# Kernel tuning notes

Hardware: AMD Instinct MI355X
Metric: run time of the kernel (lower is better)

## Reference

```python
import jax, jax.numpy as jnp
import numpy as np

D_MODEL = 128
NHEAD = 8
NLAYERS = 6
LAYER_NAMES = ['self', 'cross', 'self', 'cross', 'self', 'cross']
TEMPERATURE = 5.0
EPS = 1e-6


def _pos_encoding(x):
    # Sinusoidal 1D position encoding along the width axis. x: [N, H, W, C]
    C, W = x.shape[-1], x.shape[2]
    pos = jnp.arange(W, dtype=x.dtype)[:, None]                      # [W,1]
    div = jnp.exp(jnp.arange(0, C, 2, dtype=x.dtype) * (-np.log(10000.0) / C))
    pe = jnp.zeros((W, C), x.dtype)
    pe = pe.at[:, 0::2].set(jnp.sin(pos * div))
    pe = pe.at[:, 1::2].set(jnp.cos(pos * div))
    return x + pe[None, None]                                        # broadcast over N,H


def _linear_attention(q, k, v):
    # q,k,v: [N, H, W, nhead, dim]; kernelized linear attention along W
    Q = jax.nn.elu(q) + 1.0
    K = jax.nn.elu(k) + 1.0
    v_len = v.shape[2]
    V = v / v_len
    KV = jnp.einsum('nhsed,nhsev->nhedv', K, V)                      # [N,H,e,d,d]
    Z = 1.0 / (jnp.einsum('nhled,nhed->nhle', Q, K.sum(axis=2)) + EPS)
    return jnp.einsum('nhled,nhedv,nhle->nhlev', Q, KV, Z) * v_len


def _layer_norm(x, g, b):
    m = x.mean(-1, keepdims=True)
    v = jnp.mean((x - m) ** 2, -1, keepdims=True)
    return (x - m) / jnp.sqrt(v + 1e-5) * g + b


def _encoder_layer(x, source, Wq, Wk, Wv, Wm, W1, W2, g1, b1, g2, b2):
    x = _pos_encoding(x)
    source = _pos_encoding(source)
    bs, h, w, c = x.shape
    e, d = NHEAD, c // NHEAD
    q = (x @ Wq).reshape(bs, h, w, e, d)
    k = (source @ Wk).reshape(bs, h, w, e, d)
    v = (source @ Wv).reshape(bs, h, w, e, d)
    msg = _linear_attention(q, k, v).reshape(bs, h, w, c) @ Wm
    msg = _layer_norm(msg, g1, b1)
    msg = jnp.concatenate([x, msg], axis=-1)                         # [N,H,W,2C]
    msg = jax.nn.relu(msg @ W1) @ W2
    msg = _layer_norm(msg, g2, b2)
    return x + msg


def _forward(feat0, feat1, Wq, Wk, Wv, Wm, W1, W2, g1, b1, g2, b2):
    feat0 = feat0.transpose(0, 2, 3, 1)                              # [N,H,W,C]
    feat1 = feat1.transpose(0, 2, 3, 1)
    for i, name in enumerate(LAYER_NAMES):
        p = (Wq[i], Wk[i], Wv[i], Wm[i], W1[i], W2[i], g1[i], b1[i], g2[i], b2[i])
        if name == 'self':
            feat0 = _encoder_layer(feat0, feat0, *p)
            feat1 = _encoder_layer(feat1, feat1, *p)
        else:  # cross: sequential update (feat1 sees updated feat0), as in torch source
            feat0 = _encoder_layer(feat0, feat1, *p)
            feat1 = _encoder_layer(feat1, feat0, *p)
    w = feat0.shape[2]
    attn_mask = jnp.where(jnp.triu(jnp.ones((w, w), bool), 1), -jnp.inf, 0.0)
    attn_mask = attn_mask[None, None].astype(feat0.dtype)
    scale = feat0.shape[-1] ** 0.5
    sim = jnp.einsum('ntwc,ntlc->ntwl', feat0 / scale, feat1 / scale) / TEMPERATURE
    return sim + attn_mask


def setup_inputs() -> dict:
    key = jax.random.key(0)
    ks = jax.random.split(key, 12)
    N, C, H, W = 2, D_MODEL, 64, 640
    L, D = NLAYERS, D_MODEL
    s = 1.0 / np.sqrt(D)
    s2 = 1.0 / np.sqrt(2 * D)
    return {
        'feat0': jax.random.normal(ks[0], (N, C, H, W), jnp.float32),
        'feat1': jax.random.normal(ks[1], (N, C, H, W), jnp.float32),
        'Wq': jax.random.normal(ks[2], (L, D, D), jnp.float32) * s,
        'Wk': jax.random.normal(ks[3], (L, D, D), jnp.float32) * s,
        'Wv': jax.random.normal(ks[4], (L, D, D), jnp.float32) * s,
        'Wm': jax.random.normal(ks[5], (L, D, D), jnp.float32) * s,
        'W1': jax.random.normal(ks[6], (L, 2 * D, 2 * D), jnp.float32) * s2,
        'W2': jax.random.normal(ks[7], (L, 2 * D, D), jnp.float32) * s2,
        'g1': jnp.ones((L, D), jnp.float32),
        'b1': jnp.zeros((L, D), jnp.float32),
        'g2': jnp.ones((L, D), jnp.float32),
        'b2': jnp.zeros((L, D), jnp.float32),
    }


def reference(feat0, feat1, Wq, Wk, Wv, Wm, W1, W2, g1, b1, g2, b2):
    return _forward(feat0, feat1, Wq, Wk, Wv, Wm, W1, W2, g1, b1, g2, b2)
```

## Files before the change

kernel.cpp:

```cpp
#include <hip/hip_runtime.h>
#include <cmath>
#include <math.h>

#define TOK 81920
#define WDIM 640

typedef __attribute__((ext_vector_type(8))) short short8v;
typedef __attribute__((ext_vector_type(4))) short short4v;
typedef __attribute__((ext_vector_type(4))) float f32x4;

__device__ __forceinline__ short f2bf(float f) {
  union { float f; unsigned u; } x; x.f = f;
  unsigned r = (x.u + 0x7fffu + ((x.u >> 16) & 1u)) >> 16;
  return (short)r;
}
__device__ __forceinline__ float bf2f(short s) {
  union { unsigned u; float f; } x; x.u = ((unsigned)(unsigned short)s) << 16;
  return x.f;
}

__global__ __launch_bounds__(256) void pe_kernel(float* __restrict__ pe) {
  int id = blockIdx.x * 256 + threadIdx.x;
  if (id >= WDIM * 128) return;
  int w = id >> 7;
  int c = id & 127;
  float i2 = (float)(c & 126);
  float freq = expf(i2 * -0.071955784156063941f);
  float ang = (float)w * freq;
  pe[id] = (c & 1) ? cosf(ang) : sinf(ang);
}

__global__ __launch_bounds__(256) void tr_kernel(const float* __restrict__ in0,
                                                 const float* __restrict__ in1,
                                                 short* __restrict__ x0,
                                                 short* __restrict__ x1) {
  __shared__ float t[32][33];
  int w0 = blockIdx.x * 32;
  int c0 = blockIdx.y * 32;
  int z = blockIdx.z;
  int feat = z >> 7;
  int nh = z & 127;
  int n = nh >> 6, h = nh & 63;
  const float* in = feat ? in1 : in0;
  short* out = feat ? x1 : x0;
  int tx = threadIdx.x & 31, ty = threadIdx.x >> 5;
  const float* ip = in + ((n * 128 + c0) * 64 + h) * 640 + w0;
#pragma unroll
  for (int i = 0; i < 32; i += 8)
    t[ty + i][tx] = ip[(ty + i) * (64 * 640) + tx];
  __syncthreads();
  short* op = out + ((size_t)(n * 64 + h) * 640 + w0) * 128 + c0;
#pragma unroll
  for (int i = 0; i < 32; i += 8)
    op[(size_t)(ty + i) * 128 + tx] = f2bf(t[tx][ty + i]);
}

__global__ __launch_bounds__(256) void wprep_kernel(
    const float* __restrict__ Wq, const float* __restrict__ Wk,
    const float* __restrict__ Wv, const float* __restrict__ Wm,
    const float* __restrict__ W1, const float* __restrict__ W2,
    short* __restrict__ BT) {
  int id = blockIdx.x * 256 + threadIdx.x;
  if (id >= 6 * 163840) return;
  int layer = id / 163840;
  int r = id % 163840;
  float v;
  if (r < 65536) {
    int seg = r >> 14;
    int rr = r & 16383;
    int n = rr >> 7, k = rr & 127;
    const float* W = seg == 0 ? Wq : seg == 1 ? Wk : seg == 2 ? Wv : Wm;
    v = W[layer * 16384 + k * 128 + n];
  } else if (r < 131072) {
    int rr = r - 65536;
    int n = rr >> 8, k = rr & 255;
    v = W1[layer * 65536 + k * 256 + n];
  } else {
    int rr = r - 131072;
    int n = rr >> 8, k = rr & 255;
    v = W2[layer * 32768 + k * 128 + n];
  }
  BT[id] = f2bf(v);
}

__device__ __forceinline__ void load_af(const short* __restrict__ A,
                                        const float* __restrict__ pe,
                                        int bm, int wr, int l15, int lk,
                                        short8v af[4][4]) {
  const int wbase = bm % WDIM;
#pragma unroll
  for (int mf = 0; mf < 4; ++mf) {
    const int rl = wr * 64 + mf * 16 + l15;
    const short* ar = A + (size_t)(bm + rl) * 128;
    const float* pr = pe + (size_t)(wbase + rl) * 128;
#pragma unroll
    for (int ks = 0; ks < 4; ++ks) {
      const int kloc = ks * 32 + lk * 8;
      short8v xa = *(const short8v*)(ar + kloc);
      f32x4 p0 = *(const f32x4*)(pr + kloc);
      f32x4 p1 = *(const f32x4*)(pr + kloc + 4);
      short8v o;
      o[0] = f2bf(bf2f(xa[0]) + p0[0]); o[1] = f2bf(bf2f(xa[1]) + p0[1]);
      o[2] = f2bf(bf2f(xa[2]) + p0[2]); o[3] = f2bf(bf2f(xa[3]) + p0[3]);
      o[4] = f2bf(bf2f(xa[4]) + p1[0]); o[5] = f2bf(bf2f(xa[5]) + p1[1]);
      o[6] = f2bf(bf2f(xa[6]) + p1[2]); o[7] = f2bf(bf2f(xa[7]) + p1[3]);
      af[ks][mf] = o;
    }
  }
}

__device__ __forceinline__ void proj_pass_T(const short8v af[4][4],
                                            const short* __restrict__ WT,
                                            int wr, int wc, int l15, int lk,
                                            short (*tS)[136]) {
  f32x4 acc[4][4] = {};
#pragma unroll
  for (int ks = 0; ks < 4; ++ks) {
    const int kloc = ks * 32 + lk * 8;
    short8v bfr[4];
#pragma unroll
    for (int nf = 0; nf < 4; ++nf)
      bfr[nf] = *(const short8v*)&WT[(size_t)(wc * 64 + nf * 16 + l15) * 128 + kloc];
#pragma unroll
    for (int mf = 0; mf < 4; ++mf)
#pragma unroll
      for (int nf = 0; nf < 4; ++nf)
        acc[mf][nf] = __builtin_amdgcn_mfma_f32_16x16x32_bf16(
            bfr[nf], af[ks][mf], acc[mf][nf], 0, 0, 0);
  }
#pragma unroll
  for (int mf = 0; mf < 4; ++mf)
#pragma unroll
    for (int nf = 0; nf < 4; ++nf) {
      short4v p;
      p[0] = f2bf(acc[mf][nf][0]); p[1] = f2bf(acc[mf][nf][1]);
      p[2] = f2bf(acc[mf][nf][2]); p[3] = f2bf(acc[mf][nf][3]);
      *(short4v*)&tS[wr * 64 + mf * 16 + l15][wc * 64 + nf * 16 + lk * 4] = p;
    }
}

__device__ __forceinline__ void tile_out(const short (*tS)[136], int bm, int tid,
                                         short* __restrict__ out) {
#pragma unroll
  for (int it = 0; it < 8; ++it) {
    int u = it * 256 + tid;
    int row = u >> 4, seg = u & 15;
    *(short8v*)&out[(size_t)(bm + row) * 128 + seg * 8] =
        *(const short8v*)&tS[row][seg * 8];
  }
}

__global__ __launch_bounds__(256) void qkv_self_kernel(
    const short* __restrict__ x0, const short* __restrict__ x1,
    const float* __restrict__ pe,
    const short* __restrict__ wqT, const short* __restrict__ wkT,
    const short* __restrict__ wvT,
    short* q0, short* k0, short* v0, short* q1, short* k1, short* v1) {
  __shared__ short tS[128][136];
  const int tid = threadIdx.x, lane = tid & 63, wid = tid >> 6;
  const int wr = wid >> 1, wc = wid & 1;
  const int bm = blockIdx.x * 128;
  const int l15 = lane & 15, lk = lane >> 4;
  const int z = blockIdx.z;
  const short* A = z ? x1 : x0;
  short8v af[4][4];
  load_af(A, pe, bm, wr, l15, lk, af);
  proj_pass_T(af, wqT, wr, wc, l15, lk, tS);
  __syncthreads();
  tile_out(tS, bm, tid, z ? q1 : q0);
  __syncthreads();
  proj_pass_T(af, wkT, wr, wc, l15, lk, tS);
  __syncthreads();
  tile_out(tS, bm, tid, z ? k1 : k0);
  __syncthreads();
  proj_pass_T(af, wvT, wr, wc, l15, lk, tS);
  __syncthreads();
  tile_out(tS, bm, tid, z ? v1 : v0);
}

__global__ __launch_bounds__(256) void qkv_cross_kernel(
    const short* __restrict__ xq, const short* __restrict__ xs,
    const float* __restrict__ pe,
    const short* __restrict__ wqT, const short* __restrict__ wkT,
    const short* __restrict__ wvT,
    short* qb, short* kb, short* vb) {
  __shared__ short tS[128][136];
  const int tid = threadIdx.x, lane = tid & 63, wid = tid >> 6;
  const int wr = wid >> 1, wc = wid & 1;
  const int bm = blockIdx.x * 128;
  const int l15 = lane & 15, lk = lane >> 4;
  short8v af[4][4];
  if (blockIdx.y == 0) {
    load_af(xq, pe, bm, wr, l15, lk, af);
    proj_pass_T(af, wqT, wr, wc, l15, lk, tS);
    __syncthreads();
    tile_out(tS, bm, tid, qb);
  } else {
    load_af(xs, pe, bm, wr, l15, lk, af);
    proj_pass_T(af, wkT, wr, wc, l15, lk, tS);
    __syncthreads();
    tile_out(tS, bm, tid, kb);
    __syncthreads();
    proj_pass_T(af, wvT, wr, wc, l15, lk, tS);
    __syncthreads();
    tile_out(tS, bm, tid, vb);
  }
}

template <int NSC>
__global__ __launch_bounds__(256) void kv_kernel(
    const short* __restrict__ k0, const short* __restrict__ v0,
    const short* __restrict__ k1, const short* __restrict__ v1,
    float* __restrict__ kvp) {
  const int bid = blockIdx.x;
  const int sc = bid % NSC;
  const int e = bid / NSC;
  const int strip = sc / 5, chunk = sc % 5;
  const short* kb = (strip >= 128) ? k1 : k0;
  const short* vb = (strip >= 128) ? v1 : v0;
  const int nh = strip & 127;
  const size_t base = (size_t)nh * (640 * 128) + (size_t)chunk * (128 * 128) + e * 16;
  __shared__ float Ks[128][16];
  __shared__ float Vs[128][16];
  const int tid = threadIdx.x;
  const int srow = tid >> 1, shalf = (tid & 1) * 8;
  short8v k8 = *(const short8v*)&kb[base + (size_t)srow * 128 + shalf];
  short8v v8 = *(const short8v*)&vb[base + (size_t)srow * 128 + shalf];
#pragma unroll
  for (int j = 0; j < 8; ++j) {
    float kr = bf2f(k8[j]);
    Ks[srow][shalf + j] = kr > 0.f ? kr + 1.f : __expf(kr);
    Vs[srow][shalf + j] = bf2f(v8[j]);
  }
  __syncthreads();
  const int d = tid >> 4, vv = tid & 15;
  float kv = 0.f, ks = 0.f;
#pragma unroll 8
  for (int sl = 0; sl < 128; ++sl) {
    float kk = Ks[sl][d];
    kv = fmaf(kk, Vs[sl][vv], kv);
    ks += kk;
  }
  float* out = kvp + ((size_t)(strip * 8 + e) * 5 + chunk) * 272;
  out[d * 16 + vv] = kv;
  if (vv == 0) out[256 + d] = ks;
}

template <int DUAL>
__global__ __launch_bounds__(256) void apply_wm_kernel(
    short* q0, short* q1, const float* __restrict__ kvp,
    const short* __restrict__ wmT,
    const float* __restrict__ g, const float* __restrict__ b) {
  const int bid = blockIdx.x;
  const int strip = bid / 10, lc = bid % 10;
  __shared__ float KV8[8][16][17];
  __shared__ float KS8[8][16];
  __shared__ short oS[64][136];
  const int tid = threadIdx.x;
  for (int idx = tid; idx < 8 * 272; idx += 256) {
    int e = idx / 272, r = idx - e * 272;
    const float* p = kvp + ((size_t)(strip * 8 + e) * 5) * 272 + r;
    float s = ((p[0] + p[272]) + (p[544] + p[816])) + p[1088];
    if (r < 256) KV8[e][r >> 4][r & 15] = s;
    else         KS8[e][r - 256] = s;
  }
  __syncthreads();
  short* qb = (DUAL && strip >= 128) ? q1 : q0;
  const int nh = strip & 127;
  const int lrow = tid >> 2;
  const int row = lc * 64 + lrow;
  const int cb = (tid & 3) * 32;
  short* qp = qb + (size_t)nh * (640 * 128) + (size_t)row * 128 + cb;
  short8v qv0 = *(const short8v*)(qp);
  short8v qv1 = *(const short8v*)(qp + 8);
  short8v qv2 = *(const short8v*)(qp + 16);
  short8v qv3 = *(const short8v*)(qp + 24);
  float qe[32];
#pragma unroll
  for (int j = 0; j < 8; ++j) {
    float a = bf2f(qv0[j]); qe[j]      = a > 0.f ? a + 1.f : __expf(a);
    float c1 = bf2f(qv1[j]); qe[8 + j]  = c1 > 0.f ? c1 + 1.f : __expf(c1);
    float c2 = bf2f(qv2[j]); qe[16 + j] = c2 > 0.f ? c2 + 1.f : __expf(c2);
    float c3 = bf2f(qv3[j]); qe[24 + j] = c3 > 0.f ? c3 + 1.f : __expf(c3);
  }
  short res[32];
#pragma unroll
  for (int h = 0; h < 2; ++h) {
    const int e = (cb >> 4) + h;
    const float* Q = qe + h * 16;
    float dz = 0.f;
#pragma unroll
    for (int dd = 0; dd < 16; ++dd) dz = fmaf(Q[dd], KS8[e][dd], dz);
    const float zi = 1.f / (dz + 1e-6f);
#pragma unroll
    for (int vv = 0; vv < 16; ++vv) {
      float o = 0.f;
#pragma unroll
      for (int dd = 0; dd < 16; ++dd) o = fmaf(Q[dd], KV8[e][dd][vv], o);
      res[h * 16 + vv] = f2bf(o * zi);
    }
  }
  short8v w0, w1, w2, w3;
#pragma unroll
  for (int j = 0; j < 8; ++j) {
    w0[j] = res[j]; w1[j] = res[8 + j]; w2[j] = res[16 + j]; w3[j] = res[24 + j];
  }
  *(short8v*)&oS[lrow][cb]      = w0;
  *(short8v*)&oS[lrow][cb + 8]  = w1;
  *(short8v*)&oS[lrow][cb + 16] = w2;
  *(short8v*)&oS[lrow][cb + 24] = w3;
  __syncthreads();
  const int lane = tid & 63, wv = tid >> 6;
  const int l15 = lane & 15, lk = lane >> 4;
  f32x4 acc[8] = {};
#pragma unroll
  for (int ks = 0; ks < 4; ++ks) {
    const int kloc = ks * 32 + lk * 8;
    short8v afr = *(const short8v*)&oS[wv * 16 + l15][kloc];
    short8v bfr[8];
#pragma unroll
    for (int nf = 0; nf < 8; ++nf)
      bfr[nf] = *(const short8v*)&wmT[(size_t)(nf * 16 + l15) * 128 + kloc];
#pragma unroll
    for (int nf = 0; nf < 8; ++nf)
      acc[nf] = __builtin_amdgcn_mfma_f32_16x16x32_bf16(bfr[nf], afr, acc[nf], 0, 0, 0);
  }
  float s = 0.f, qq = 0.f;
#pragma unroll
  for (int nf = 0; nf < 8; ++nf)
#pragma unroll
    for (int r = 0; r < 4; ++r) {
      s += acc[nf][r];
      qq = fmaf(acc[nf][r], acc[nf][r], qq);
    }
  s += __shfl_xor(s, 16);  qq += __shfl_xor(qq, 16);
  s += __shfl_xor(s, 32);  qq += __shfl_xor(qq, 32);
  float mean = s * (1.f / 128.f);
  float var = qq * (1.f / 128.f) - mean * mean;
  float rstd = rsqrtf(var + 1e-5f);
#pragma unroll
  for (int nf = 0; nf < 8; ++nf) {
    f32x4 g4 = *(const f32x4*)&g[nf * 16 + lk * 4];
    f32x4 b4 = *(const f32x4*)&b[nf * 16 + lk * 4];
    short4v p;
#pragma unroll
    for (int r = 0; r < 4; ++r)
      p[r] = f2bf((acc[nf][r] - mean) * rstd * g4[r] + b4[r]);
    *(short4v*)&oS[wv * 16 + l15][nf * 16 + lk * 4] = p;
  }
  __syncthreads();
  short* mp = qb + (size_t)nh * (640 * 128) + (size_t)(lc * 64) * 128;
#pragma unroll
  for (int it = 0; it < 4; ++it) {
    int u = it * 256 + tid;
    int rw = u >> 4, seg = u & 15;
    *(short8v*)&mp[(size_t)rw * 128 + seg * 8] = *(const short8v*)&oS[rw][seg * 8];
  }
}

__global__ __launch_bounds__(256) void w1_kernel(
    const short* __restrict__ xA, const short* __restrict__ xB,
    const short* __restrict__ mA, const short* __restrict__ mB,
    const float* __restrict__ pe, const short* __restrict__ w1T,
    short* h0A, short* h1A, short* h0B, short* h1B) {
  __shared__ short tS[128][136];
  const int z = blockIdx.z;
  const short* x = z ? xB : xA;
  const short* m = z ? mB : mA;
  short* h0 = z ? h0B : h0A;
  short* h1 = z ? h1B : h1A;
  const int tid = threadIdx.x, lane = tid & 63, wid = tid >> 6;
  const int wr = wid >> 1, wc = wid & 1;
  const int bm = blockIdx.x * 128;
  const int l15 = lane & 15, lk = lane >> 4;
  const int wbase = bm % WDIM;
  for (int p = 0; p < 2; ++p) {
    f32x4 acc[4][4] = {};
#pragma unroll
    for (int ks = 0; ks < 8; ++ks) {
      const int kloc = ks * 32 + lk * 8;
      short8v bfr[4], afr[4];
#pragma unroll
      for (int nf = 0; nf < 4; ++nf)
        bfr[nf] = *(const short8v*)&w1T[(size_t)(p * 128 + wc * 64 + nf * 16 + l15) * 256 + kloc];
      if (ks < 4) {
#pragma unroll
        for (int mf = 0; mf < 4; ++mf) {
          const int rl = wr * 64 + mf * 16 + l15;
          short8v xa = *(const short8v*)(x + (size_t)(bm + rl) * 128 + kloc);
          const float* pr = pe + (size_t)(wbase + rl) * 128 + kloc;
          f32x4 p0 = *(const f32x4*)pr;
          f32x4 p1 = *(const f32x4*)(pr + 4);
          short8v ov;
          ov[0] = f2bf(bf2f(xa[0]) + p0[0]); ov[1] = f2bf(bf2f(xa[1]) + p0[1]);
          ov[2] = f2bf(bf2f(xa[2]) + p0[2]); ov[3] = f2bf(bf2f(xa[3]) + p0[3]);
          ov[4] = f2bf(bf2f(xa[4]) + p1[0]); ov[5] = f2bf(bf2f(xa[5]) + p1[1]);
          ov[6] = f2bf(bf2f(xa[6]) + p1[2]); ov[7] = f2bf(bf2f(xa[7]) + p1[3]);
          afr[mf] = ov;
        }
      } else {
#pragma unroll
        for (int mf = 0; mf < 4; ++mf)
          afr[mf] = *(const short8v*)&m[(size_t)(bm + wr * 64 + mf * 16 + l15) * 128 + kloc - 128];
      }
#pragma unroll
      for (int mf = 0; mf < 4; ++mf)
#pragma unroll
        for (int nf = 0; nf < 4; ++nf)
          acc[mf][nf] = __builtin_amdgcn_mfma_f32_16x16x32_bf16(
              bfr[nf], afr[mf], acc[mf][nf], 0, 0, 0);
    }
#pragma unroll
    for (int mf = 0; mf < 4; ++mf)
#pragma unroll
      for (int nf = 0; nf < 4; ++nf) {
        short4v pk;
#pragma unroll
        for (int r = 0; r < 4; ++r)
          pk[r] = f2bf(fmaxf(acc[mf][nf][r], 0.f));
        *(short4v*)&tS[wr * 64 + mf * 16 + l15][wc * 64 + nf * 16 + lk * 4] = pk;
      }
    __syncthreads();
    tile_out(tS, bm, tid, p ? h1 : h0);
    __syncthreads();
  }
}

__global__ __launch_bounds__(256) void w2_ln_kernel(
    const short* __restrict__ h0A, const short* __restrict__ h1A,
    const short* __restrict__ h0B, const short* __restrict__ h1B,
    const short* __restrict__ w2T, short* xA, short* xB,
    const float* __restrict__ pe, const float* __restrict__ g,
    const float* __restrict__ b) {
  __shared__ short tS[128][136];
  __shared__ float lds_s[2][128];
  __shared__ float lds_q[2][128];
  const int z = blockIdx.z;
  const short* h0 = z ? h0B : h0A;
  const short* h1 = z ? h1B : h1A;
  short* x = z ? xB : xA;
  const int tid = threadIdx.x, lane = tid & 63, wid = tid >> 6;
  const int wr = wid >> 1, wc = wid & 1;
  const int bm = blockIdx.x * 128;
  const int l15 = lane & 15, lk = lane >> 4;
  const int wbase = bm % WDIM;
  f32x4 acc[4][4] = {};
#pragma unroll
  for (int ks = 0; ks < 8; ++ks) {
    const int kloc = ks * 32 + lk * 8;
    const short* hp = (ks < 4) ? h0 : h1;
    const int kl = (ks < 4) ? kloc : kloc - 128;
    short8v bfr[4], afr[4];
#pragma unroll
    for (int nf = 0; nf < 4; ++nf)
      bfr[nf] = *(const short8v*)&w2T[(size_t)(wc * 64 + nf * 16 + l15) * 256 + kloc];
#pragma unroll
    for (int mf = 0; mf < 4; ++mf)
      afr[mf] = *(const short8v*)&hp[(size_t)(bm + wr * 64 + mf * 16 + l15) * 128 + kl];
#pragma unroll
    for (int mf = 0; mf < 4; ++mf)
#pragma unroll
      for (int nf = 0; nf < 4; ++nf)
        acc[mf][nf] = __builtin_amdgcn_mfma_f32_16x16x32_bf16(
            bfr[nf], afr[mf], acc[mf][nf], 0, 0, 0);
  }
#pragma unroll
  for (int mf = 0; mf < 4; ++mf) {
    float s = 0.f, qq = 0.f;
#pragma unroll
    for (int nf = 0; nf < 4; ++nf)
#pragma unroll
      for (int r = 0; r < 4; ++r) {
        s += acc[mf][nf][r];
        qq = fmaf(acc[mf][nf][r], acc[mf][nf][r], qq);
      }
    s += __shfl_xor(s, 16);  qq += __shfl_xor(qq, 16);
    s += __shfl_xor(s, 32);  qq += __shfl_xor(qq, 32);
    if (lk == 0) {
      int rl = wr * 64 + mf * 16 + l15;
      lds_s[wc][rl] = s;
      lds_q[wc][rl] = qq;
    }
  }
  __syncthreads();
#pragma unroll
  for (int mf = 0; mf < 4; ++mf) {
    int rl = wr * 64 + mf * 16 + l15;
    float mean = (lds_s[0][rl] + lds_s[1][rl]) * (1.f / 128.f);
    float var = (lds_q[0][rl] + lds_q[1][rl]) * (1.f / 128.f) - mean * mean;
    float rstd = rsqrtf(var + 1e-5f);
#pragma unroll
    for (int nf = 0; nf < 4; ++nf) {
      f32x4 g4 = *(const f32x4*)&g[wc * 64 + nf * 16 + lk * 4];
      f32x4 b4 = *(const f32x4*)&b[wc * 64 + nf * 16 + lk * 4];
      short4v pk;
#pragma unroll
      for (int r = 0; r < 4; ++r)
        pk[r] = f2bf((acc[mf][nf][r] - mean) * rstd * g4[r] + b4[r]);
      *(short4v*)&tS[rl][wc * 64 + nf * 16 + lk * 4] = pk;
    }
  }
  __syncthreads();
#pragma unroll
  for (int it = 0; it < 8; ++it) {
    int u = it * 256 + tid;
    int row = u >> 4, seg = u & 15;
    size_t xi = (size_t)(bm + row) * 128 + seg * 8;
    short8v xv8 = *(const short8v*)&x[xi];
    short8v t8 = *(const short8v*)&tS[row][seg * 8];
    const float* pr = pe + (size_t)(wbase + row) * 128 + seg * 8;
    f32x4 p0 = *(const f32x4*)pr;
    f32x4 p1 = *(const f32x4*)(pr + 4);
    short8v o8;
    o8[0] = f2bf(bf2f(xv8[0]) + p0[0] + bf2f(t8[0]));
    o8[1] = f2bf(bf2f(xv8[1]) + p0[1] + bf2f(t8[1]));
    o8[2] = f2bf(bf2f(xv8[2]) + p0[2] + bf2f(t8[2]));
    o8[3] = f2bf(bf2f(xv8[3]) + p0[3] + bf2f(t8[3]));
    o8[4] = f2bf(bf2f(xv8[4]) + p1[0] + bf2f(t8[4]));
    o8[5] = f2bf(bf2f(xv8[5]) + p1[1] + bf2f(t8[5]));
    o8[6] = f2bf(bf2f(xv8[6]) + p1[2] + bf2f(t8[6]));
    o8[7] = f2bf(bf2f(xv8[7]) + p1[3] + bf2f(t8[7]));
    *(short8v*)&x[xi] = o8;
  }
}

__global__ __launch_bounds__(256) void sim_mfma(const short* __restrict__ f0,
                                                const short* __restrict__ f1,
                                                float* __restrict__ out) {
  const int fid = (blockIdx.z * 5 + blockIdx.y) * 5 + blockIdx.x;
  const int c8 = fid & 7, kk_ = fid >> 3;
  const int nt = c8 * 16 + kk_ / 25;
  const int r2 = kk_ % 25;
  const int bw = (r2 % 5) * 128;
  const int bl = (r2 / 5) * 128;
  const int tid = threadIdx.x;
  const int lane = tid & 63;
  const int wid = tid >> 6;
  const int wr = wid >> 1, wc = wid & 1;
  const short* __restrict__ A = f0 + (size_t)nt * 640 * 128;
  const short* __restrict__ B = f1 + (size_t)nt * 640 * 128;
  const int l15 = lane & 15;
  const int lk = lane >> 4;
  f32x4 acc[4][4] = {};
#pragma unroll
  for (int ks = 0; ks < 4; ++ks) {
    const int kloc = ks * 32 + lk * 8;
    short8v afr[4], bfr[4];
#pragma unroll
    for (int mf = 0; mf < 4; ++mf)
      afr[mf] = *(const short8v*)&A[(size_t)(bw + wr * 64 + mf * 16 + l15) * 128 + kloc];
#pragma unroll
    for (int nf = 0; nf < 4; ++nf)
      bfr[nf] = *(const short8v*)&B[(size_t)(bl + wc * 64 + nf * 16 + l15) * 128 + kloc];
#pragma unroll
    for (int mf = 0; mf < 4; ++mf)
#pragma unroll
      for (int nf = 0; nf < 4; ++nf)
        acc[mf][nf] = __builtin_amdgcn_mfma_f32_16x16x32_bf16(
            afr[mf], bfr[nf], acc[mf][nf], 0, 0, 0);
  }
#pragma unroll
  for (int mf = 0; mf < 4; ++mf)
#pragma unroll
    for (int nf = 0; nf < 4; ++nf) {
      const int l = bl + wc * 64 + nf * 16 + l15;
#pragma unroll
      for (int r = 0; r < 4; ++r) {
        const int w = bw + wr * 64 + mf * 16 + lk * 4 + r;
        float v = acc[mf][nf][r] * (1.f / 640.f);
        if (l > w) v = -1e30f;
        out[((size_t)nt * 640 + w) * 640 + l] = v;
      }
    }
}

extern "C" void kernel_launch(void* const* d_in, const int* in_sizes, int n_in,
                              void* d_out, int out_size, void* d_ws, size_t ws_size,
                              hipStream_t stream) {
  (void)in_sizes; (void)n_in; (void)out_size; (void)ws_size;
  const float* feat0 = (const float*)d_in[0];
  const float* feat1 = (const float*)d_in[1];
  const float* Wq = (const float*)d_in[2];
  const float* Wk = (const float*)d_in[3];
  const float* Wv = (const float*)d_in[4];
  const float* Wm = (const float*)d_in[5];
  const float* W1 = (const float*)d_in[6];
  const float* W2 = (const float*)d_in[7];
  const float* g1 = (const float*)d_in[8];
  const float* b1 = (const float*)d_in[9];
  const float* g2 = (const float*)d_in[10];
  const float* b2 = (const float*)d_in[11];

  float* wsf = (float*)d_ws;
  const size_t U = (size_t)TOK * 128;
  float* pe = wsf;
  short* x0 = (short*)(wsf + 81920);
  short* x1 = x0 + U;
  short* q0 = x1 + U;
  short* k0 = q0 + U;
  short* v0 = k0 + U;
  short* q1 = v0 + U;
  short* k1 = q1 + U;
  short* v1 = k1 + U;
  short* bt = v1 + U;
  float* kvp = (float*)(bt + 983040);

  dim3 blk(256);
  pe_kernel<<<dim3(320), blk, 0, stream>>>(pe);
  tr_kernel<<<dim3(20, 4, 256), blk, 0, stream>>>(feat0, feat1, x0, x1);
  wprep_kernel<<<dim3((6 * 163840 + 255) / 256), blk, 0, stream>>>(
      Wq, Wk, Wv, Wm, W1, W2, bt);

  const int NB = TOK / 128;
  for (int i = 0; i < 6; ++i) {
    const short* bt_i = bt + (size_t)i * 163840;
    const short* wqT = bt_i;
    const short* wkT = bt_i + 16384;
    const short* wvT = bt_i + 32768;
    const short* wmT = bt_i + 49152;
    const short* w1T = bt_i + 65536;
    const short* w2T = bt_i + 131072;
    const float* g1_i = g1 + i * 128;
    const float* b1_i = b1 + i * 128;
    const float* g2_i = g2 + i * 128;
    const float* b2_i = b2 + i * 128;
    if ((i & 1) == 0) {
      qkv_self_kernel<<<dim3(NB, 1, 2), blk, 0, stream>>>(
          x0, x1, pe, wqT, wkT, wvT, q0, k0, v0, q1, k1, v1);
      kv_kernel<1280><<<dim3(8 * 1280), blk, 0, stream>>>(k0, v0, k1, v1, kvp);
      apply_wm_kernel<1><<<dim3(2560), blk, 0, stream>>>(q0, q1, kvp, wmT, g1_i, b1_i);
      w1_kernel<<<dim3(NB, 1, 2), blk, 0, stream>>>(
          x0, x1, q0, q1, pe, w1T, k0, v0, k1, v1);
      w2_ln_kernel<<<dim3(NB, 1, 2), blk, 0, stream>>>(
          k0, v0, k1, v1, w2T, x0, x1, pe, g2_i, b2_i);
    } else {
      qkv_cross_kernel<<<dim3(NB, 2), blk, 0, stream>>>(
          x0, x1, pe, wqT, wkT, wvT, q0, k0, v0);
      kv_kernel<640><<<dim3(8 * 640), blk, 0, stream>>>(k0, v0, k0, v0, kvp);
      apply_wm_kernel<0><<<dim3(1280), blk, 0, stream>>>(q0, q0, kvp, wmT, g1_i, b1_i);
      w1_kernel<<<dim3(NB, 1, 1), blk, 0, stream>>>(
          x0, x0, q0, q0, pe, w1T, k0, v0, k0, v0);
      w2_ln_kernel<<<dim3(NB, 1, 1), blk, 0, stream>>>(
          k0, v0, k0, v0, w2T, x0, x0, pe, g2_i, b2_i);

      qkv_cross_kernel<<<dim3(NB, 2), blk, 0, stream>>>(
          x1, x0, pe, wqT, wkT, wvT, q0, k0, v0);
      kv_kernel<640><<<dim3(8 * 640), blk, 0, stream>>>(k0, v0, k0, v0, kvp);
      apply_wm_kernel<0><<<dim3(1280), blk, 0, stream>>>(q0, q0, kvp, wmT, g1_i, b1_i);
      w1_kernel<<<dim3(NB, 1, 1), blk, 0, stream>>>(
          x1, x1, q0, q0, pe, w1T, k0, v0, k0, v0);
      w2_ln_kernel<<<dim3(NB, 1, 1), blk, 0, stream>>>(
          k0, v0, k0, v0, w2T, x1, x1, pe, g2_i, b2_i);
    }
  }
  sim_mfma<<<dim3(5, 5, 128), blk, 0, stream>>>(x0, x1, (float*)d_out);
}
```

Baseline: 2.487 ms.

## Fuse KV reduction into QKV projection kernel, skip K/V global writes

The K/V projection epilogue now applies the elu+1 feature map and keeps K and V tiles in shared memory. Each block then computes the per-chunk KV and K-sum partials directly into kvp, which removes the separate kv_kernel launch and the global write and re-read of K and V. The cost is doubled shared memory per block (two 128x136 bf16 tiles), which may reduce occupancy. It also adds a serial 8-head reduction loop per block that reads bf16 from LDS.

```diff
diff --git a/kernel.cpp b/kernel.cpp
--- a/kernel.cpp
+++ b/kernel.cpp
@@ -109,6 +109,7 @@
   }
 }
 
+template <int OP>
 __device__ __forceinline__ void proj_pass_T(const short8v af[4][4],
                                             const short* __restrict__ WT,
                                             int wr, int wc, int l15, int lk,
@@ -133,8 +134,12 @@
 #pragma unroll
     for (int nf = 0; nf < 4; ++nf) {
       short4v p;
-      p[0] = f2bf(acc[mf][nf][0]); p[1] = f2bf(acc[mf][nf][1]);
-      p[2] = f2bf(acc[mf][nf][2]); p[3] = f2bf(acc[mf][nf][3]);
+#pragma unroll
+      for (int r = 0; r < 4; ++r) {
+        float t = acc[mf][nf][r];
+        if (OP == 1) t = t > 0.f ? t + 1.f : __expf(t);
+        p[r] = f2bf(t);
+      }
       *(short4v*)&tS[wr * 64 + mf * 16 + l15][wc * 64 + nf * 16 + lk * 4] = p;
     }
 }
@@ -150,32 +155,53 @@
   }
 }
 
+__device__ __forceinline__ void kv_reduce(const short (*tSk)[136],
+                                          const short (*tSv)[136],
+                                          int strip, int chunk, int tid,
+                                          float* __restrict__ kvp) {
+  const int d = tid >> 4, vv = tid & 15;
+#pragma unroll
+  for (int e = 0; e < 8; ++e) {
+    float kv = 0.f, ks = 0.f;
+#pragma unroll 8
+    for (int s = 0; s < 128; ++s) {
+      float kk = bf2f(tSk[s][e * 16 + d]);
+      kv = fmaf(kk, bf2f(tSv[s][e * 16 + vv]), kv);
+      ks += kk;
+    }
+    float* out = kvp + ((size_t)(strip * 8 + e) * 5 + chunk) * 272;
+    out[d * 16 + vv] = kv;
+    if (vv == 0) out[256 + d] = ks;
+  }
+}
+
 __global__ __launch_bounds__(256) void qkv_self_kernel(
     const short* __restrict__ x0, const short* __restrict__ x1,
     const float* __restrict__ pe,
     const short* __restrict__ wqT, const short* __restrict__ wkT,
     const short* __restrict__ wvT,
-    short* q0, short* k0, short* v0, short* q1, short* k1, short* v1) {
-  __shared__ short tS[128][136];
+    short* q0, short* q1, float* __restrict__ kvp) {
+  __shared__ short tSa[128][136];
+  __shared__ short tSb[128][136];
   const int tid = threadIdx.x, lane = tid & 63, wid = tid >> 6;
   const int wr = wid >> 1, wc = wid & 1;
   const int bm = blockIdx.x * 128;
   const int l15 = lane & 15, lk = lane >> 4;
   const int z = blockIdx.z;
+  const int nh = bm / WDIM;
+  const int chunk = (bm % WDIM) >> 7;
+  const int strip = z * 128 + nh;
   const short* A = z ? x1 : x0;
   short8v af[4][4];
   load_af(A, pe, bm, wr, l15, lk, af);
-  proj_pass_T(af, wqT, wr, wc, l15, lk, tS);
-  __syncthreads();
-  tile_out(tS, bm, tid, z ? q1 : q0);
-  __syncthreads();
-  proj_pass_T(af, wkT, wr, wc, l15, lk, tS);
-  __syncthreads();
-  tile_out(tS, bm, tid, z ? k1 : k0);
-  __syncthreads();
-  proj_pass_T(af, wvT, wr, wc, l15, lk, tS);
-  __syncthreads();
-  tile_out(tS, bm, tid, z ? v1 : v0);
+  proj_pass_T<0>(af, wqT, wr, wc, l15, lk, tSb);
+  __syncthreads();
+  tile_out(tSb, bm, tid, z ? q1 : q0);
+  __syncthreads();
+  proj_pass_T<1>(af, wkT, wr, wc, l15, lk, tSb);
+  proj_pass_T<0>(af, wvT, wr, wc, l15, lk, tSa);
+  __syncthreads();
+  kv_reduce(tSb, tSa, strip, chunk, tid, kvp);
 }
 
 __global__ __launch_bounds__(256) void qkv_cross_kernel(
@@ -183,67 +209,28 @@
     const float* __restrict__ pe,
     const short* __restrict__ wqT, const short* __restrict__ wkT,
     const short* __restrict__ wvT,
-    short* qb, short* kb, short* vb) {
-  __shared__ short tS[128][136];
+    short* qb, float* __restrict__ kvp) {
+  __shared__ short tSa[128][136];
+  __shared__ short tSb[128][136];
   const int tid = threadIdx.x, lane = tid & 63, wid = tid >> 6;
   const int wr = wid >> 1, wc = wid & 1;
   const int bm = blockIdx.x * 128;
   const int l15 = lane & 15, lk = lane >> 4;
+  const int nh = bm / WDIM;
+  const int chunk = (bm % WDIM) >> 7;
   short8v af[4][4];
   if (blockIdx.y == 0) {
     load_af(xq, pe, bm, wr, l15, lk, af);
-    proj_pass_T(af, wqT, wr, wc, l15, lk, tS);
+    proj_pass_T<0>(af, wqT, wr, wc, l15, lk, tSb);
     __syncthreads();
-    tile_out(tS, bm, tid, qb);
+    tile_out(tSb, bm, tid, qb);
   } else {
     load_af(xs, pe, bm, wr, l15, lk, af);
-    proj_pass_T(af, wkT, wr, wc, l15, lk, tS);
+    proj_pass_T<1>(af, wkT, wr, wc, l15, lk, tSb);
+    proj_pass_T<0>(af, wvT, wr, wc, l15, lk, tSa);
     __syncthreads();
-    tile_out(tS, bm, tid, kb);
-    __syncthreads();
-    proj_pass_T(af, wvT, wr, wc, l15, lk, tS);
-    __syncthreads();
-    tile_out(tS, bm, tid, vb);
-  }
-}
-
-template <int NSC>
-__global__ __launch_bounds__(256) void kv_kernel(
-    const short* __restrict__ k0, const short* __restrict__ v0,
-    const short* __restrict__ k1, const short* __restrict__ v1,
-    float* __restrict__ kvp) {
-  const int bid = blockIdx.x;
-  const int sc = bid % NSC;
-  const int e = bid / NSC;
-  const int strip = sc / 5, chunk = sc % 5;
-  const short* kb = (strip >= 128) ? k1 : k0;
-  const short* vb = (strip >= 128) ? v1 : v0;
-  const int nh = strip & 127;
-  const size_t base = (size_t)nh * (640 * 128) + (size_t)chunk * (128 * 128) + e * 16;
-  __shared__ float Ks[128][16];
-  __shared__ float Vs[128][16];
-  const int tid = threadIdx.x;
-  const int srow = tid >> 1, shalf = (tid & 1) * 8;
-  short8v k8 = *(const short8v*)&kb[base + (size_t)srow * 128 + shalf];
-  short8v v8 = *(const short8v*)&vb[base + (size_t)srow * 128 + shalf];
-#pragma unroll
-  for (int j = 0; j < 8; ++j) {
-    float kr = bf2f(k8[j]);
-    Ks[srow][shalf + j] = kr > 0.f ? kr + 1.f : __expf(kr);
-    Vs[srow][shalf + j] = bf2f(v8[j]);
-  }
-  __syncthreads();
-  const int d = tid >> 4, vv = tid & 15;
-  float kv = 0.f, ks = 0.f;
-#pragma unroll 8
-  for (int sl = 0; sl < 128; ++sl) {
-    float kk = Ks[sl][d];
-    kv = fmaf(kk, Vs[sl][vv], kv);
-    ks += kk;
-  }
-  float* out = kvp + ((size_t)(strip * 8 + e) * 5 + chunk) * 272;
-  out[d * 16 + vv] = kv;
-  if (vv == 0) out[256 + d] = ks;
+    kv_reduce(tSb, tSa, nh, chunk, tid, kvp);
+  }
 }
 
 template <int DUAL>
@@ -626,8 +613,7 @@
     const float* b2_i = b2 + i * 128;
     if ((i & 1) == 0) {
       qkv_self_kernel<<<dim3(NB, 1, 2), blk, 0, stream>>>(
-          x0, x1, pe, wqT, wkT, wvT, q0, k0, v0, q1, k1, v1);
-      kv_kernel<1280><<<dim3(8 * 1280), blk, 0, stream>>>(k0, v0, k1, v1, kvp);
+          x0, x1, pe, wqT, wkT, wvT, q0, q1, kvp);
       apply_wm_kernel<1><<<dim3(2560), blk, 0, stream>>>(q0, q1, kvp, wmT, g1_i, b1_i);
       w1_kernel<<<dim3(NB, 1, 2), blk, 0, stream>>>(
           x0, x1, q0, q1, pe, w1T, k0, v0, k1, v1);
@@ -635,8 +621,7 @@
           k0, v0, k1, v1, w2T, x0, x1, pe, g2_i, b2_i);
     } else {
       qkv_cross_kernel<<<dim3(NB, 2), blk, 0, stream>>>(
-          x0, x1, pe, wqT, wkT, wvT, q0, k0, v0);
-      kv_kernel<640><<<dim3(8 * 640), blk, 0, stream>>>(k0, v0, k0, v0, kvp);
+          x0, x1, pe, wqT, wkT, wvT, q0, kvp);
       apply_wm_kernel<0><<<dim3(1280), blk, 0, stream>>>(q0, q0, kvp, wmT, g1_i, b1_i);
       w1_kernel<<<dim3(NB, 1, 1), blk, 0, stream>>>(
           x0, x0, q0, q0, pe, w1T, k0, v0, k0, v0);
@@ -644,8 +629,7 @@
           k0, v0, k0, v0, w2T, x0, x0, pe, g2_i, b2_i);
 
       qkv_cross_kernel<<<dim3(NB, 2), blk, 0, stream>>>(
-          x1, x0, pe, wqT, wkT, wvT, q0, k0, v0);
-      kv_kernel<640><<<dim3(8 * 640), blk, 0, stream>>>(k0, v0, k0, v0, kvp);
+          x1, x0, pe, wqT, wkT, wvT, q0, kvp);
       apply_wm_kernel<0><<<dim3(1280), blk, 0, stream>>>(q0, q0, kvp, wmT, g1_i, b1_i);
       w1_kernel<<<dim3(NB, 1, 1), blk, 0, stream>>>(
           x1, x1, q0, q0, pe, w1T, k0, v0, k0, v0);
```

Result: slower. 2.796 ms (+12.4%).
